# Kernel optimization log

Hardware: AMD Instinct MI355X
Metric: run time of the kernel (lower is better)

## Reference

```python
import jax, jax.numpy as jnp
import numpy as np

B, S, E, H, WIN = 2, 4096, 768, 12, 256
D = E // H


def layer_norm(x, g, b, eps=1e-5):
    m = jnp.mean(x, axis=-1, keepdims=True)
    v = jnp.mean((x - m) ** 2, axis=-1, keepdims=True)
    return (x - m) * jax.lax.rsqrt(v + eps) * g + b


def sliding_window_attention(q, k, v, w):
    """Exact symmetric banded attention (Longformer sliding_chunks): each query
    attends to keys in [i-w, i+w], edges masked to -inf (autoregressive=False).
    q,k,v: (B,H,S,D). Returns (B,H,S,D)."""
    b, h, s, d = q.shape
    nb = s // w  # number of query blocks of width w
    q = q * (1.0 / jnp.sqrt(jnp.asarray(d, q.dtype)))
    qb = q.reshape(b, h, nb, w, d)

    def blocks3(t):
        # overlapping key/value blocks of length 3w with stride w (zero halo pad)
        tp = jnp.pad(t, ((0, 0), (0, 0), (w, w), (0, 0)))
        tw = tp.reshape(b, h, nb + 2, w, d)
        return jnp.concatenate([tw[:, :, 0:nb], tw[:, :, 1:nb + 1], tw[:, :, 2:nb + 2]], axis=3)  # (B,H,nb,3w,D)

    kb = blocks3(k)
    vb = blocks3(v)

    # (B,H,nb,w,3w): query block c local x vs key window local y (global j = c*w - w + y)
    scores = jnp.einsum('bhcxd,bhcyd->bhcxy', qb, kb)

    x_idx = jnp.arange(w)[:, None]            # (w,1) local query pos
    y_idx = jnp.arange(3 * w)[None, :]        # (1,3w) local key pos
    diag_ok = (y_idx >= x_idx) & (y_idx <= x_idx + 2 * w)   # |j - i| <= w
    c_idx = jnp.arange(nb)[:, None, None]     # (nb,1,1)
    j = c_idx * w - w + y_idx[None]           # (nb,1,3w) global key index
    in_seq = (j >= 0) & (j < s)
    mask = diag_ok[None] & in_seq             # (nb,w,3w)

    neg = jnp.finfo(scores.dtype).min
    scores = jnp.where(mask[None, None], scores, neg)
    p = jax.nn.softmax(scores, axis=-1)
    out = jnp.einsum('bhcxy,bhcyd->bhcxd', p, vb)
    return out.reshape(b, h, s, d)


def setup_inputs() -> dict:
    key = jax.random.key(0)
    ks = jax.random.split(key, 6)
    std = 0.02
    return {
        'x': jax.random.normal(ks[0], (B, S, E), jnp.float32),
        'ln1_g': jnp.ones((E,), jnp.float32),
        'ln1_b': jnp.zeros((E,), jnp.float32),
        'c_attn_w': jax.random.normal(ks[1], (E, 3 * E), jnp.float32) * std,
        'c_attn_b': jnp.zeros((3 * E,), jnp.float32),
        'c_proj_w': jax.random.normal(ks[2], (E, E), jnp.float32) * std,
        'c_proj_b': jnp.zeros((E,), jnp.float32),
        'ln2_g': jnp.ones((E,), jnp.float32),
        'ln2_b': jnp.zeros((E,), jnp.float32),
        'fc_w': jax.random.normal(ks[3], (E, 4 * E), jnp.float32) * std,
        'fc_b': jnp.zeros((4 * E,), jnp.float32),
        'proj2_w': jax.random.normal(ks[4], (4 * E, E), jnp.float32) * std,
        'proj2_b': jnp.zeros((E,), jnp.float32),
        'w': WIN,
    }


def reference(x, ln1_g, ln1_b, c_attn_w, c_attn_b, c_proj_w, c_proj_b,
              ln2_g, ln2_b, fc_w, fc_b, proj2_w, proj2_b, w):
    b, s, e = x.shape
    h = layer_norm(x, ln1_g, ln1_b)
    qkv = h @ c_attn_w + c_attn_b                 # (B,S,3E)
    q, k, v = jnp.split(qkv, 3, axis=-1)
    q = q.reshape(b, s, H, D).transpose(0, 2, 1, 3)
    k = k.reshape(b, s, H, D).transpose(0, 2, 1, 3)
    v = v.reshape(b, s, H, D).transpose(0, 2, 1, 3)
    a = sliding_window_attention(q, k, v, int(w))  # (B,H,S,D)
    a = a.transpose(0, 2, 1, 3).reshape(b, s, e)
    x = x + a @ c_proj_w + c_proj_b
    h2 = layer_norm(x, ln2_g, ln2_b)
    ff = jax.nn.gelu(h2 @ fc_w + fc_b, approximate=False)
    x = x + ff @ proj2_w + proj2_b
    return x
```

## Files before the change

kernel.cpp:

```cpp
#include <hip/hip_runtime.h>
#include <cstdint>
#include <cstddef>

typedef unsigned short US;
typedef __attribute__((ext_vector_type(8))) short bf16x8_t;
typedef __attribute__((ext_vector_type(4))) float f32x4_t;
typedef __attribute__((ext_vector_type(4))) int   i32x4_t;
typedef __attribute__((ext_vector_type(2))) unsigned int u32x2_t;

__device__ __forceinline__ float bf2f(US u) {
  union { unsigned int i; float f; } c; c.i = ((unsigned int)u) << 16; return c.f;
}
__device__ __forceinline__ US f2bf(float f) {
  union { float f; unsigned int i; } c; c.f = f;
  unsigned int i = c.i;
  return (US)((i + 0x7fffu + ((i >> 16) & 1u)) >> 16);
}

__device__ __forceinline__ void async16(const US* g, US* l) {
  __builtin_amdgcn_global_load_lds((const __attribute__((address_space(1))) void*)g,
                                   (__attribute__((address_space(3))) void*)l,
                                   16, 0, 0);
}

__device__ __forceinline__ float gelu_exact(float v) {
  float y = fabsf(v) * 0.70710678118654752f;
  float t = 1.0f / (1.0f + 0.3275911f * y);
  float poly = ((((1.061405429f * t - 1.453152027f) * t + 1.421413741f) * t
                 - 0.284496736f) * t + 0.254829592f) * t;
  float erfv = 1.0f - poly * __expf(-y * y);
  erfv = copysignf(erfv, v);
  return 0.5f * v * (1.0f + erfv);
}

__global__ __launch_bounds__(256) void ln_kernel(const float* __restrict__ x,
                                                 const float* __restrict__ g,
                                                 const float* __restrict__ b,
                                                 US* __restrict__ out) {
  int wv = threadIdx.x >> 6, lane = threadIdx.x & 63;
  long row = (long)blockIdx.x * 4 + wv;
  const float* xr = x + row * 768 + lane * 12;
  f32x4_t d0 = *(const f32x4_t*)(xr);
  f32x4_t d1 = *(const f32x4_t*)(xr + 4);
  f32x4_t d2 = *(const f32x4_t*)(xr + 8);
  float v[12] = {d0[0], d0[1], d0[2], d0[3], d1[0], d1[1], d1[2], d1[3],
                 d2[0], d2[1], d2[2], d2[3]};
  float s = 0.f, sq = 0.f;
  for (int k = 0; k < 12; k++) { s += v[k]; sq += v[k]*v[k]; }
  for (int m = 1; m < 64; m <<= 1) { s += __shfl_xor(s, m, 64); sq += __shfl_xor(sq, m, 64); }
  float mean = s * (1.f/768.f);
  float var  = sq * (1.f/768.f) - mean*mean;
  float rs   = rsqrtf(var + 1e-5f);
  const float* gp = g + lane*12;
  const float* bp = b + lane*12;
  unsigned int o[6];
  for (int k = 0; k < 6; k++) {
    US r0 = f2bf((v[2*k]   - mean) * rs * gp[2*k]   + bp[2*k]);
    US r1 = f2bf((v[2*k+1] - mean) * rs * gp[2*k+1] + bp[2*k+1]);
    o[k] = (unsigned int)r0 | ((unsigned int)r1 << 16);
  }
  US* orow = out + row * 768 + lane * 12;
  *(u32x2_t*)(orow)     = (u32x2_t){o[0], o[1]};
  *(u32x2_t*)(orow + 4) = (u32x2_t){o[2], o[3]};
  *(u32x2_t*)(orow + 8) = (u32x2_t){o[4], o[5]};
}

__global__ __launch_bounds__(256) void cvtT_kernel(const float* __restrict__ in,
                                                   US* __restrict__ out,
                                                   int K, int N) {
  __shared__ float tile[32][33];
  int bx = blockIdx.x * 32;
  int by = blockIdx.y * 32;
  int tx = threadIdx.x, ty = threadIdx.y;
  for (int i = ty; i < 32; i += 8) tile[i][tx] = in[(long)(by + i) * N + bx + tx];
  __syncthreads();
  for (int i = ty; i < 32; i += 8) out[(long)(bx + i) * K + by + tx] = f2bf(tile[tx][i]);
}

template <int EPI, int OUTBF>
__global__ __launch_bounds__(256) void gemm_bt(const US* __restrict__ A,
                                               const US* __restrict__ Bt,
                                               const float* __restrict__ bias,
                                               const float* __restrict__ res,
                                               void* __restrict__ Cv,
                                               int M, int N, int K) {
  __shared__ US As0[128 * 32];
  __shared__ US As1[128 * 32];
  __shared__ US Bs0[128 * 32];
  __shared__ US Bs1[128 * 32];
  const int tid  = threadIdx.x;
  const int lane = tid & 63;
  const int wv   = tid >> 6;
  const int quad = lane >> 4;
  const int l15  = lane & 15;
  const int wm   = (wv >> 1) * 64;
  const int wn   = (wv & 1) * 64;
  const long bm  = (long)blockIdx.x * 128;
  const long bn  = (long)blockIdx.y * 128;

  const int srow  = wv * 16 + (lane >> 2);
  const int skoff = (lane & 3) * 8;
  const US* Ag  = A  + (bm + srow) * (long)K + skoff;
  const US* Ag2 = Ag + 64 * (long)K;
  const US* Bg  = Bt + (bn + srow) * (long)K + skoff;
  const US* Bg2 = Bg + 64 * (long)K;
  US* a0l = As0 + wv * 512;   US* a0l2 = As0 + 2048 + wv * 512;
  US* a1l = As1 + wv * 512;   US* a1l2 = As1 + 2048 + wv * 512;
  US* b0l = Bs0 + wv * 512;   US* b0l2 = Bs0 + 2048 + wv * 512;
  US* b1l = Bs1 + wv * 512;   US* b1l2 = Bs1 + 2048 + wv * 512;

  f32x4_t acc[4][4] = {};

  for (int k0 = 0; k0 < K; k0 += 64) {
    __syncthreads();
    async16(Ag  + k0,      a0l);
    async16(Ag2 + k0,      a0l2);
    async16(Ag  + k0 + 32, a1l);
    async16(Ag2 + k0 + 32, a1l2);
    async16(Bg  + k0,      b0l);
    async16(Bg2 + k0,      b0l2);
    async16(Bg  + k0 + 32, b1l);
    async16(Bg2 + k0 + 32, b1l2);
    __syncthreads();
    {
      bf16x8_t af[4], bfr[4];
      for (int t = 0; t < 4; t++)
        af[t]  = *(const bf16x8_t*)(As0 + (wm + t*16 + l15) * 32 + quad * 8);
      for (int t = 0; t < 4; t++)
        bfr[t] = *(const bf16x8_t*)(Bs0 + (wn + t*16 + l15) * 32 + quad * 8);
      for (int r = 0; r < 4; r++)
        for (int c = 0; c < 4; c++)
          acc[r][c] = __builtin_amdgcn_mfma_f32_16x16x32_bf16(af[r], bfr[c], acc[r][c], 0, 0, 0);
    }
    {
      bf16x8_t af[4], bfr[4];
      for (int t = 0; t < 4; t++)
        af[t]  = *(const bf16x8_t*)(As1 + (wm + t*16 + l15) * 32 + quad * 8);
      for (int t = 0; t < 4; t++)
        bfr[t] = *(const bf16x8_t*)(Bs1 + (wn + t*16 + l15) * 32 + quad * 8);
      for (int r = 0; r < 4; r++)
        for (int c = 0; c < 4; c++)
          acc[r][c] = __builtin_amdgcn_mfma_f32_16x16x32_bf16(af[r], bfr[c], acc[r][c], 0, 0, 0);
    }
  }

  US*    Cb = (US*)Cv;
  float* Cf = (float*)Cv;
  for (int c = 0; c < 4; c++) {
    long gcol = bn + wn + c*16 + l15;
    float bv = bias[gcol];
    for (int r = 0; r < 4; r++) {
      long grow0 = bm + wm + r*16 + quad*4;
      for (int i = 0; i < 4; i++) {
        long idx = (grow0 + i) * (long)N + gcol;
        float v = acc[r][c][i] + bv;
        if (EPI == 1) v += res[idx];
        if (EPI == 2) v = gelu_exact(v);
        if (OUTBF) Cb[idx] = f2bf(v);
        else       Cf[idx] = v;
      }
    }
  }
}

template <int EPI, int OUTBF>
__global__ __launch_bounds__(256) void gemm_kn(const US* __restrict__ A,
                                               const float* __restrict__ B,
                                               const float* __restrict__ bias,
                                               const float* __restrict__ res,
                                               void* __restrict__ Cv,
                                               int M, int N, int K) {
  __shared__ US As[128 * 48];
  __shared__ US Bs[128 * 48];
  const int tid  = threadIdx.x;
  const int lane = tid & 63;
  const int wv   = tid >> 6;
  const int quad = lane >> 4;
  const int l15  = lane & 15;
  const int wm   = (wv >> 1) * 64;
  const int wn   = (wv & 1) * 64;
  const long bm  = (long)blockIdx.x * 128;
  const long bn  = (long)blockIdx.y * 128;

  const int srow = tid >> 1;
  const int scol = (tid & 1) * 16;
  const US* Ag = A + (bm + srow) * (long)K + scol;
  US* Asw = As + srow * 48 + scol;
  const float* Bg = B + bn + lane;

  f32x4_t acc[4][4] = {};

  for (int k0 = 0; k0 < K; k0 += 32) {
    i32x4_t a0 = *(const i32x4_t*)(Ag + k0);
    i32x4_t a1 = *(const i32x4_t*)(Ag + k0 + 8);
    unsigned int bv0[4], bv1[4];
    for (int kp = 0; kp < 4; kp++) {
      long rof = (long)(k0 + wv * 8 + kp * 2) * N;
      US lo0 = f2bf(Bg[rof]);
      US hi0 = f2bf(Bg[rof + N]);
      US lo1 = f2bf(Bg[rof + 64]);
      US hi1 = f2bf(Bg[rof + N + 64]);
      bv0[kp] = (unsigned int)lo0 | ((unsigned int)hi0 << 16);
      bv1[kp] = (unsigned int)lo1 | ((unsigned int)hi1 << 16);
    }
    __syncthreads();
    *(i32x4_t*)(Asw)     = a0;
    *(i32x4_t*)(Asw + 8) = a1;
    for (int kp = 0; kp < 4; kp++) {
      *(unsigned int*)(Bs + lane * 48 + wv * 8 + kp * 2)        = bv0[kp];
      *(unsigned int*)(Bs + (64 + lane) * 48 + wv * 8 + kp * 2) = bv1[kp];
    }
    __syncthreads();
    bf16x8_t af[4], bfr[4];
    for (int t = 0; t < 4; t++)
      af[t]  = *(const bf16x8_t*)(As + (wm + t*16 + l15) * 48 + quad * 8);
    for (int t = 0; t < 4; t++)
      bfr[t] = *(const bf16x8_t*)(Bs + (wn + t*16 + l15) * 48 + quad * 8);
    for (int r = 0; r < 4; r++)
      for (int c = 0; c < 4; c++)
        acc[r][c] = __builtin_amdgcn_mfma_f32_16x16x32_bf16(af[r], bfr[c], acc[r][c], 0, 0, 0);
  }

  US*    Cb = (US*)Cv;
  float* Cf = (float*)Cv;
  for (int c = 0; c < 4; c++) {
    long gcol = bn + wn + c*16 + l15;
    float bv = bias[gcol];
    for (int r = 0; r < 4; r++) {
      long grow0 = bm + wm + r*16 + quad*4;
      for (int i = 0; i < 4; i++) {
        long idx = (grow0 + i) * (long)N + gcol;
        float v = acc[r][c][i] + bv;
        if (EPI == 1) v += res[idx];
        if (EPI == 2) v = gelu_exact(v);
        if (OUTBF) Cb[idx] = f2bf(v);
        else       Cf[idx] = v;
      }
    }
  }
}

__global__ __launch_bounds__(256) void attn_kernel(const US* __restrict__ qkv,
                                                   US* __restrict__ aout) {
  __shared__ US Qs [64 * 72];
  __shared__ US Ks [64 * 72];
  __shared__ US Vts[64 * 74];
  __shared__ US Ps [4 * 16 * 72];

  const int tid  = threadIdx.x;
  const int lane = tid & 63;
  const int wv   = tid >> 6;
  const int quad = lane >> 4;
  const int l15  = lane & 15;

  const int qt = blockIdx.x & 63;
  const int hh = (blockIdx.x >> 6) % 12;
  const int bb = blockIdx.x / (64 * 12);
  const int q0 = qt * 64;
  const long tokbase = (long)bb * 4096;
  const int qoff = hh * 64;
  const int koff = 768 + qoff;
  const int voff = 1536 + qoff;

  for (int it = 0; it < 2; it++) {
    int idx = tid + it * 256;
    int r = idx >> 3, part = (idx & 7) * 8;
    i32x4_t d = *(const i32x4_t*)(qkv + (tokbase + q0 + r) * 2304 + qoff + part);
    *(i32x4_t*)(Qs + r * 72 + part) = d;
  }
  __syncthreads();
  bf16x8_t aq0 = *(const bf16x8_t*)(Qs + (wv*16 + l15) * 72 + quad * 8);
  bf16x8_t aq1 = *(const bf16x8_t*)(Qs + (wv*16 + l15) * 72 + 32 + quad * 8);

  bf16x8_t ones;
  for (int j = 0; j < 8; j++) ones[j] = (short)0x3F80;

  f32x4_t O[4] = {};
  f32x4_t lacc = {};
  const float sc2 = 0.125f * 1.4426950408889634f;
  const int qrow0 = q0 + wv*16 + quad*4;

  for (int t = 0; t < 9; t++) {
    const int kt0 = q0 - 256 + t * 64;
    if (kt0 + 63 < 0 || kt0 >= 4096) continue;
    const bool edge = (t == 0) || (t == 8) || (kt0 < 0) || (kt0 + 63 >= 4096);
    __syncthreads();
    for (int it = 0; it < 2; it++) {
      int idx = tid + it * 256;
      int r = idx >> 3, part = (idx & 7) * 8;
      int kg = kt0 + r;
      bool in = (kg >= 0 && kg < 4096);
      i32x4_t dk = {}, dv = {};
      if (in) {
        const US* base = qkv + (tokbase + kg) * 2304;
        dk = *(const i32x4_t*)(base + koff + part);
        dv = *(const i32x4_t*)(base + voff + part);
      }
      *(i32x4_t*)(Ks + r * 72 + part) = dk;
      alignas(16) US tmp[8];
      *(i32x4_t*)tmp = dv;
      for (int j = 0; j < 8; j++)
        Vts[(part + j) * 74 + r] = tmp[j];
    }
    __syncthreads();

    float p[4][4];
    for (int c = 0; c < 4; c++) {
      bf16x8_t bk0 = *(const bf16x8_t*)(Ks + (c*16 + l15) * 72 + quad * 8);
      bf16x8_t bk1 = *(const bf16x8_t*)(Ks + (c*16 + l15) * 72 + 32 + quad * 8);
      f32x4_t z = {};
      z = __builtin_amdgcn_mfma_f32_16x16x32_bf16(aq0, bk0, z, 0, 0, 0);
      z = __builtin_amdgcn_mfma_f32_16x16x32_bf16(aq1, bk1, z, 0, 0, 0);
      if (edge) {
        int kglob = kt0 + c*16 + l15;
        bool kin = (kglob >= 0) && (kglob < 4096);
        for (int i = 0; i < 4; i++) {
          int qg = qrow0 + i;
          bool ok = kin && (kglob >= qg - 256) && (kglob <= qg + 256);
          p[c][i] = ok ? exp2f(fminf(z[i] * sc2, 60.f)) : 0.f;
        }
      } else {
        for (int i = 0; i < 4; i++)
          p[c][i] = exp2f(fminf(z[i] * sc2, 60.f));
      }
    }
    for (int c = 0; c < 4; c++)
      for (int i = 0; i < 4; i++)
        Ps[wv*1152 + (quad*4 + i) * 72 + c*16 + l15] = f2bf(p[c][i]);
    bf16x8_t ap0 = *(const bf16x8_t*)(Ps + wv*1152 + l15 * 72 + quad * 8);
    bf16x8_t ap1 = *(const bf16x8_t*)(Ps + wv*1152 + l15 * 72 + 32 + quad * 8);
    for (int c2 = 0; c2 < 4; c2++) {
      bf16x8_t bv0 = *(const bf16x8_t*)(Vts + (c2*16 + l15) * 74 + quad * 8);
      bf16x8_t bv1 = *(const bf16x8_t*)(Vts + (c2*16 + l15) * 74 + 32 + quad * 8);
      O[c2] = __builtin_amdgcn_mfma_f32_16x16x32_bf16(ap0, bv0, O[c2], 0, 0, 0);
      O[c2] = __builtin_amdgcn_mfma_f32_16x16x32_bf16(ap1, bv1, O[c2], 0, 0, 0);
    }
    lacc = __builtin_amdgcn_mfma_f32_16x16x32_bf16(ap0, ones, lacc, 0, 0, 0);
    lacc = __builtin_amdgcn_mfma_f32_16x16x32_bf16(ap1, ones, lacc, 0, 0, 0);
  }

  for (int c2 = 0; c2 < 4; c2++)
    for (int i = 0; i < 4; i++) {
      long tok = tokbase + q0 + wv*16 + quad*4 + i;
      aout[tok * 768 + qoff + c2*16 + l15] = f2bf(O[c2][i] / lacc[i]);
    }
}

extern "C" void kernel_launch(void* const* d_in, const int* in_sizes, int n_in,
                              void* d_out, int out_size, void* d_ws, size_t ws_size,
                              hipStream_t stream) {
  const float* x        = (const float*)d_in[0];
  const float* ln1_g    = (const float*)d_in[1];
  const float* ln1_b    = (const float*)d_in[2];
  const float* c_attn_w = (const float*)d_in[3];
  const float* c_attn_b = (const float*)d_in[4];
  const float* c_proj_w = (const float*)d_in[5];
  const float* c_proj_b = (const float*)d_in[6];
  const float* ln2_g    = (const float*)d_in[7];
  const float* ln2_b    = (const float*)d_in[8];
  const float* fc_w     = (const float*)d_in[9];
  const float* fc_b     = (const float*)d_in[10];
  const float* proj2_w  = (const float*)d_in[11];
  const float* proj2_b  = (const float*)d_in[12];

  US*    hba = (US*)d_ws;
  US*    qkv = hba + 8192L * 768;
  US*    ff  = qkv;
  float* x1  = (float*)d_out;
  float* out = (float*)d_out;

  const size_t FAST_NEED = 77070336;
  if (ws_size >= FAST_NEED) {
    US* wqkvT = (US*)((char*)d_ws + 62914560);
    US* wprjT = wqkvT + 2304L * 768;
    US* wfcT  = wprjT + 768L * 768;
    US* wp2T  = wfcT  + 3072L * 768;
    dim3 tb(32, 8);
    cvtT_kernel<<<dim3(2304/32,  768/32), tb, 0, stream>>>(c_attn_w, wqkvT, 768, 2304);
    cvtT_kernel<<<dim3( 768/32,  768/32), tb, 0, stream>>>(c_proj_w, wprjT, 768,  768);
    cvtT_kernel<<<dim3(3072/32,  768/32), tb, 0, stream>>>(fc_w,     wfcT,  768, 3072);
    cvtT_kernel<<<dim3( 768/32, 3072/32), tb, 0, stream>>>(proj2_w,  wp2T, 3072,  768);

    ln_kernel<<<2048, 256, 0, stream>>>(x, ln1_g, ln1_b, hba);
    gemm_bt<0,1><<<dim3(64, 18), 256, 0, stream>>>(hba, wqkvT, c_attn_b, nullptr,
                                                   qkv, 8192, 2304, 768);
    attn_kernel<<<1536, 256, 0, stream>>>(qkv, hba);
    gemm_bt<1,0><<<dim3(64, 6), 256, 0, stream>>>(hba, wprjT, c_proj_b, x,
                                                  x1, 8192, 768, 768);
    ln_kernel<<<2048, 256, 0, stream>>>(x1, ln2_g, ln2_b, hba);
    gemm_bt<2,1><<<dim3(64, 24), 256, 0, stream>>>(hba, wfcT, fc_b, nullptr,
                                                   ff, 8192, 3072, 768);
    gemm_bt<1,0><<<dim3(64, 6), 256, 0, stream>>>(ff, wp2T, proj2_b, x1,
                                                  out, 8192, 768, 3072);
  } else {
    ln_kernel<<<2048, 256, 0, stream>>>(x, ln1_g, ln1_b, hba);
    gemm_kn<0,1><<<dim3(64, 18), 256, 0, stream>>>(hba, c_attn_w, c_attn_b, nullptr,
                                                   qkv, 8192, 2304, 768);
    attn_kernel<<<1536, 256, 0, stream>>>(qkv, hba);
    gemm_kn<1,0><<<dim3(64, 6), 256, 0, stream>>>(hba, c_proj_w, c_proj_b, x,
                                                  x1, 8192, 768, 768);
    ln_kernel<<<2048, 256, 0, stream>>>(x1, ln2_g, ln2_b, hba);
    gemm_kn<2,1><<<dim3(64, 24), 256, 0, stream>>>(hba, fc_w, fc_b, nullptr,
                                                   ff, 8192, 3072, 768);
    gemm_kn<1,0><<<dim3(64, 6), 256, 0, stream>>>(ff, proj2_w, proj2_b, x1,
                                                  out, 8192, 768, 3072);
  }
}
```

Baseline: 398.0 us.

## Merge weight transposes into one launch and use 128x64 tiles for N=768 GEMMs

The four weight convert-transpose launches are merged into a single kernel that picks its matrix from the block index, which saves launch overhead. The two N=768 projection GEMMs (attention projection and MLP down-projection) move to a new 128x64-tile kernel. That doubles the grid from 384 to 768 blocks so more of the MI355X compute units get work. Each block now reuses less A data per tile and the A matrix is read twice as often.

```diff
diff --git a/kernel.cpp b/kernel.cpp
--- a/kernel.cpp
+++ b/kernel.cpp
@@ -65,12 +65,19 @@
   *(u32x2_t*)(orow + 8) = (u32x2_t){o[4], o[5]};
 }
 
-__global__ __launch_bounds__(256) void cvtT_kernel(const float* __restrict__ in,
-                                                   US* __restrict__ out,
-                                                   int K, int N) {
+__global__ __launch_bounds__(256) void cvtT_all(const float* __restrict__ w0, US* __restrict__ o0,
+                                                const float* __restrict__ w1, US* __restrict__ o1,
+                                                const float* __restrict__ w2, US* __restrict__ o2,
+                                                const float* __restrict__ w3, US* __restrict__ o3) {
   __shared__ float tile[32][33];
-  int bx = blockIdx.x * 32;
-  int by = blockIdx.y * 32;
+  int bid = blockIdx.x;
+  const float* in; US* out; int K, N, nx, rel;
+  if (bid < 1728)      { in = w0; out = o0; K = 768;  N = 2304; nx = 72; rel = bid; }
+  else if (bid < 2304) { in = w1; out = o1; K = 768;  N = 768;  nx = 24; rel = bid - 1728; }
+  else if (bid < 4608) { in = w2; out = o2; K = 768;  N = 3072; nx = 96; rel = bid - 2304; }
+  else                 { in = w3; out = o3; K = 3072; N = 768;  nx = 24; rel = bid - 4608; }
+  int bx = (rel % nx) * 32;
+  int by = (rel / nx) * 32;
   int tx = threadIdx.x, ty = threadIdx.y;
   for (int i = ty; i < 32; i += 8) tile[i][tx] = in[(long)(by + i) * N + bx + tx];
   __syncthreads();
@@ -163,6 +170,81 @@
   }
 }
 
+__global__ __launch_bounds__(256) void gemm_bt_n64(const US* __restrict__ A,
+                                                   const US* __restrict__ Bt,
+                                                   const float* __restrict__ bias,
+                                                   const float* __restrict__ res,
+                                                   float* __restrict__ C,
+                                                   int M, int N, int K) {
+  __shared__ US As0[128 * 32];
+  __shared__ US As1[128 * 32];
+  __shared__ US Bs0[64 * 32];
+  __shared__ US Bs1[64 * 32];
+  const int tid  = threadIdx.x;
+  const int lane = tid & 63;
+  const int wv   = tid >> 6;
+  const int quad = lane >> 4;
+  const int l15  = lane & 15;
+  const int wm   = wv * 32;
+  const long bm  = (long)blockIdx.x * 128;
+  const long bn  = (long)blockIdx.y * 64;
+
+  const int srow  = wv * 16 + (lane >> 2);
+  const int skoff = (lane & 3) * 8;
+  const US* Ag  = A  + (bm + srow) * (long)K + skoff;
+  const US* Ag2 = Ag + 64 * (long)K;
+  const US* Bg  = Bt + (bn + srow) * (long)K + skoff;
+  US* a0l = As0 + wv * 512;   US* a0l2 = As0 + 2048 + wv * 512;
+  US* a1l = As1 + wv * 512;   US* a1l2 = As1 + 2048 + wv * 512;
+  US* b0l = Bs0 + wv * 512;
+  US* b1l = Bs1 + wv * 512;
+
+  f32x4_t acc[2][4] = {};
+
+  for (int k0 = 0; k0 < K; k0 += 64) {
+    __syncthreads();
+    async16(Ag  + k0,      a0l);
+    async16(Ag2 + k0,      a0l2);
+    async16(Ag  + k0 + 32, a1l);
+    async16(Ag2 + k0 + 32, a1l2);
+    async16(Bg  + k0,      b0l);
+    async16(Bg  + k0 + 32, b1l);
+    __syncthreads();
+    {
+      bf16x8_t af[2], bfr[4];
+      for (int t = 0; t < 2; t++)
+        af[t]  = *(const bf16x8_t*)(As0 + (wm + t*16 + l15) * 32 + quad * 8);
+      for (int c = 0; c < 4; c++)
+        bfr[c] = *(const bf16x8_t*)(Bs0 + (c*16 + l15) * 32 + quad * 8);
+      for (int r = 0; r < 2; r++)
+        for (int c = 0; c < 4; c++)
+          acc[r][c] = __builtin_amdgcn_mfma_f32_16x16x32_bf16(af[r], bfr[c], acc[r][c], 0, 0, 0);
+    }
+    {
+      bf16x8_t af[2], bfr[4];
+      for (int t = 0; t < 2; t++)
+        af[t]  = *(const bf16x8_t*)(As1 + (wm + t*16 + l15) * 32 + quad * 8);
+      for (int c = 0; c < 4; c++)
+        bfr[c] = *(const bf16x8_t*)(Bs1 + (c*16 + l15) * 32 + quad * 8);
+      for (int r = 0; r < 2; r++)
+        for (int c = 0; c < 4; c++)
+          acc[r][c] = __builtin_amdgcn_mfma_f32_16x16x32_bf16(af[r], bfr[c], acc[r][c], 0, 0, 0);
+    }
+  }
+
+  for (int c = 0; c < 4; c++) {
+    long gcol = bn + c*16 + l15;
+    float bv = bias[gcol];
+    for (int r = 0; r < 2; r++) {
+      long grow0 = bm + wm + r*16 + quad*4;
+      for (int i = 0; i < 4; i++) {
+        long idx = (grow0 + i) * (long)N + gcol;
+        C[idx] = acc[r][c][i] + bv + res[idx];
+      }
+    }
+  }
+}
+
 template <int EPI, int OUTBF>
 __global__ __launch_bounds__(256) void gemm_kn(const US* __restrict__ A,
                                                const float* __restrict__ B,
@@ -375,22 +457,19 @@
     US* wprjT = wqkvT + 2304L * 768;
     US* wfcT  = wprjT + 768L * 768;
     US* wp2T  = wfcT  + 3072L * 768;
-    dim3 tb(32, 8);
-    cvtT_kernel<<<dim3(2304/32,  768/32), tb, 0, stream>>>(c_attn_w, wqkvT, 768, 2304);
-    cvtT_kernel<<<dim3( 768/32,  768/32), tb, 0, stream>>>(c_proj_w, wprjT, 768,  768);
-    cvtT_kernel<<<dim3(3072/32,  768/32), tb, 0, stream>>>(fc_w,     wfcT,  768, 3072);
-    cvtT_kernel<<<dim3( 768/32, 3072/32), tb, 0, stream>>>(proj2_w,  wp2T, 3072,  768);
+    cvtT_all<<<6912, dim3(32, 8), 0, stream>>>(c_attn_w, wqkvT, c_proj_w, wprjT,
+                                               fc_w, wfcT, proj2_w, wp2T);
 
     ln_kernel<<<2048, 256, 0, stream>>>(x, ln1_g, ln1_b, hba);
     gemm_bt<0,1><<<dim3(64, 18), 256, 0, stream>>>(hba, wqkvT, c_attn_b, nullptr,
                                                    qkv, 8192, 2304, 768);
     attn_kernel<<<1536, 256, 0, stream>>>(qkv, hba);
-    gemm_bt<1,0><<<dim3(64, 6), 256, 0, stream>>>(hba, wprjT, c_proj_b, x,
+    gemm_bt_n64<<<dim3(64, 12), 256, 0, stream>>>(hba, wprjT, c_proj_b, x,
                                                   x1, 8192, 768, 768);
     ln_kernel<<<2048, 256, 0, stream>>>(x1, ln2_g, ln2_b, hba);
     gemm_bt<2,1><<<dim3(64, 24), 256, 0, stream>>>(hba, wfcT, fc_b, nullptr,
                                                    ff, 8192, 3072, 768);
-    gemm_bt<1,0><<<dim3(64, 6), 256, 0, stream>>>(ff, wp2T, proj2_b, x1,
+    gemm_bt_n64<<<dim3(64, 12), 256, 0, stream>>>(ff, wp2T, proj2_b, x1,
                                                   out, 8192, 768, 3072);
   } else {
     ln_kernel<<<2048, 256, 0, stream>>>(x, ln1_g, ln1_b, hba);
```

Result: faster. 375.8 us (-5.6%).
